# Kernel tuning notes

Hardware: AMD Instinct MI355X
Metric: run time of the kernel (lower is better)

## Reference

```python
import jax, jax.numpy as jnp
import numpy as np

SE, SD, B = 400, 50, 32
H, IN, A = 512, 512, 128
VF, V = 1024, 32000

def _p(k, shape):
    return jax.random.normal(k, shape, dtype=jnp.float32) * 0.02

def setup_inputs() -> dict:
    key = jax.random.key(0)
    ks = jax.random.split(key, 24)
    inp = {
        'output_enc': jax.random.normal(ks[0], (SE, B, 2 * H), dtype=jnp.float32),
        'input_dec': jax.random.normal(ks[1], (SD, B, IN), dtype=jnp.float32),
        'hidden_enc': jax.random.normal(ks[2], (4, B, H), dtype=jnp.float32),
        'cell_state_enc': jax.random.normal(ks[3], (4, B, H), dtype=jnp.float32),
        # LSTM layer 0 (PyTorch gate order i,f,g,o)
        'W_ih0': _p(ks[4], (4 * H, IN)), 'W_hh0': _p(ks[5], (4 * H, H)),
        'b_ih0': _p(ks[6], (4 * H,)), 'b_hh0': _p(ks[7], (4 * H,)),
        # LSTM layer 1
        'W_ih1': _p(ks[8], (4 * H, H)), 'W_hh1': _p(ks[9], (4 * H, H)),
        'b_ih1': _p(ks[10], (4 * H,)), 'b_hh1': _p(ks[11], (4 * H,)),
        # reduce_dim: 2H -> H
        'W_red': _p(ks[12], (H, 2 * H)), 'b_red': _p(ks[13], (H,)),
        # attention: 3H -> A, attn_out: A -> 1 (no bias)
        'W_att': _p(ks[14], (A, 3 * H)), 'b_att': _p(ks[15], (A,)),
        'v_att': _p(ks[16], (1, A)),
        # vocab MLP: 3H -> VF -> V
        'W_v1': _p(ks[17], (VF, 3 * H)), 'b_v1': _p(ks[18], (VF,)),
        'W_v2': _p(ks[19], (V, VF)), 'b_v2': _p(ks[20], (V,)),
    }
    return inp

def _forward(output_enc, input_dec, hidden_enc, cell_state_enc,
             W_ih0, W_hh0, b_ih0, b_hh0, W_ih1, W_hh1, b_ih1, b_hh1,
             W_red, b_red, W_att, b_att, v_att, W_v1, b_v1, W_v2, b_v2):
    # first_word=True path: fold bidirectional encoder state [4,B,H] -> [2,B,2H] -> [2,B,H]
    old_enc = jnp.concatenate([hidden_enc[0:2], hidden_enc[2:]], axis=-1)
    old_cell = jnp.concatenate([cell_state_enc[0:2], cell_state_enc[2:]], axis=-1)
    new_enc = old_enc @ W_red.T + b_red    # [2,B,H]
    new_cell = old_cell @ W_red.T + b_red  # [2,B,H]

    def lstm_cell(x, h, c, W_ih, W_hh, b_ih, b_hh):
        g = x @ W_ih.T + h @ W_hh.T + b_ih + b_hh
        i, f, gg, o = jnp.split(g, 4, axis=-1)
        c_new = jax.nn.sigmoid(f) * c + jax.nn.sigmoid(i) * jnp.tanh(gg)
        h_new = jax.nn.sigmoid(o) * jnp.tanh(c_new)
        return h_new, c_new

    def step(carry, x_t):
        h0, c0, h1, c1 = carry
        h0, c0 = lstm_cell(x_t, h0, c0, W_ih0, W_hh0, b_ih0, b_hh0)
        h1, c1 = lstm_cell(h0, h1, c1, W_ih1, W_hh1, b_ih1, b_hh1)
        return (h0, c0, h1, c1), h1

    init = (new_enc[0], new_cell[0], new_enc[1], new_cell[1])
    (h0f, c0f, h1f, c1f), output_dec = jax.lax.scan(step, init, input_dec)
    hidden_dec = jnp.stack([h0f, h1f])       # [2,B,H]
    cell_state_dec = jnp.stack([c0f, c1f])   # [2,B,H]

    # Additive (Bahdanau) attention, batched over all decoder timesteps.
    # cat order is (output_enc, output_dec) -> first 2H cols of W_att hit encoder.
    enc_part = output_enc @ W_att[:, :2 * H].T              # [Se,B,A]
    dec_part = output_dec @ W_att[:, 2 * H:].T + b_att       # [Sd,B,A]
    e = jnp.tanh(enc_part[:, None] + dec_part[None])         # [Se,Sd,B,A]
    e = jnp.einsum('stba,a->stb', e, v_att[0])               # [Se,Sd,B]
    attn = jax.nn.softmax(e, axis=0)                         # softmax over encoder dim
    context = jnp.einsum('stb,sbe->tbe', attn, output_enc)   # [Sd,B,2H]

    pv_in = jnp.concatenate([output_dec, context], axis=-1)  # [Sd,B,3H]
    pvocab = (pv_in @ W_v1.T + b_v1) @ W_v2.T + b_v2         # [Sd,B,V]
    return pvocab, (hidden_dec, cell_state_dec)

def reference(output_enc, input_dec, hidden_enc, cell_state_enc,
              W_ih0, W_hh0, b_ih0, b_hh0, W_ih1, W_hh1, b_ih1, b_hh1,
              W_red, b_red, W_att, b_att, v_att, W_v1, b_v1, W_v2, b_v2):
    return _forward(output_enc, input_dec, hidden_enc, cell_state_enc,
                    W_ih0, W_hh0, b_ih0, b_hh0, W_ih1, W_hh1, b_ih1, b_hh1,
                    W_red, b_red, W_att, b_att, v_att, W_v1, b_v1, W_v2, b_v2)
```

## Files before the change

### kernel.cpp

```cpp
#include <hip/hip_runtime.h>
#include <cstdint>

#define DEV __device__ __forceinline__

typedef short bfrag __attribute__((ext_vector_type(8)));
typedef float ffrag __attribute__((ext_vector_type(4)));

constexpr int SE = 400, SD = 50, BB = 32;
constexpr int HH = 512, INW = 512, AA = 128;
constexpr int VF = 1024, VV = 32000;
constexpr int G4 = 2048;

DEV ushort f2bf(float f) {
    uint32_t u = __float_as_uint(f);
    u = (u + 0x7FFF + ((u >> 16) & 1)) >> 16;
    return (ushort)u;
}
DEV float bf2f(ushort u) { return __uint_as_float(((uint32_t)u) << 16); }
DEV float sigm_(float x) { return 1.f / (1.f + __expf(-x)); }
DEV float tanh_(float x) { float e = __expf(2.f * x); return 1.f - 2.f / (e + 1.f); }
DEV int imin(int a, int b) { return a < b ? a : b; }

DEV void gload_lds16(const void* g, void* l) {
    __builtin_amdgcn_global_load_lds((const __attribute__((address_space(1))) uint32_t*)g,
                                     (__attribute__((address_space(3))) uint32_t*)l, 16, 0, 0);
}

struct CvtFlatTab {
    const float* src[6];
    ushort* dst[6];
    int blk_end[6];
    int nseg;
};
__global__ __launch_bounds__(256) void k_cvt_multi(CvtFlatTab t) {
    int blk = blockIdx.x, seg = 0;
    while (seg < t.nseg - 1 && blk >= t.blk_end[seg]) seg++;
    int base = seg ? t.blk_end[seg - 1] : 0;
    long i = (long)(blk - base) * 256 + threadIdx.x;
    float4 v = ((const float4*)t.src[seg])[i];
    ushort4 o;
    o.x = f2bf(v.x); o.y = f2bf(v.y); o.z = f2bf(v.z); o.w = f2bf(v.w);
    ((ushort4*)t.dst[seg])[i] = o;
}

struct CvtStrTab {
    const float* src[4];
    ushort* dst[4];
    int ss[4], so[4], ds[4], dofs[4], c4n[4];
    int blk_end[4];
    int nseg;
};
__global__ __launch_bounds__(256) void k_cvt_str_multi(CvtStrTab t) {
    int blk = blockIdx.x, seg = 0;
    while (seg < t.nseg - 1 && blk >= t.blk_end[seg]) seg++;
    int base = seg ? t.blk_end[seg - 1] : 0;
    int i = (blk - base) * 256 + threadIdx.x;
    int c4n = t.c4n[seg];
    int r = i / c4n, c = (i - r * c4n) * 4;
    float4 v = *(const float4*)(t.src[seg] + (size_t)r * t.ss[seg] + t.so[seg] + c);
    ushort4 o;
    o.x = f2bf(v.x); o.y = f2bf(v.y); o.z = f2bf(v.z); o.w = f2bf(v.w);
    *(ushort4*)(t.dst[seg] + (size_t)r * t.ds[seg] + t.dofs[seg] + c) = o;
}

__global__ __launch_bounds__(256) void k_bsum(const float* __restrict__ bi0, const float* __restrict__ bh0,
                                              const float* __restrict__ bi1, const float* __restrict__ bh1,
                                              float* __restrict__ bsum0, float* __restrict__ bsum1) {
    int i = blockIdx.x * 256 + threadIdx.x;
    if (i >= G4) return;
    bsum0[i] = bi0[i] + bh0[i];
    bsum1[i] = bi1[i] + bh1[i];
}

__global__ __launch_bounds__(256) void k_fold(const float* __restrict__ hid,
                                              const float* __restrict__ cel,
                                              const float* __restrict__ W_red,
                                              const float* __restrict__ b_red,
                                              float* __restrict__ h0m,
                                              float* __restrict__ c0, float* __restrict__ c1,
                                              ushort* __restrict__ AB) {
    int tid = threadIdx.x;
    int j = blockIdx.x * 256 + tid;
    int b = blockIdx.y;
    int l = blockIdx.z & 1;
    bool is_c = blockIdx.z >> 1;
    const float* src = is_c ? cel : hid;
    __shared__ float xs[1024];
    for (int i = tid; i < 512; i += 256) {
        xs[i]       = src[((size_t)l * BB + b) * HH + i];
        xs[512 + i] = src[((size_t)(l + 2) * BB + b) * HH + i];
    }
    __syncthreads();
    const float4* w  = (const float4*)(W_red + (size_t)j * 1024);
    const float4* xv = (const float4*)xs;
    float acc = b_red[j];
    for (int k = 0; k < 256; k++) {
        float4 a = w[k], x = xv[k];
        acc += a.x * x.x + a.y * x.y + a.z * x.z + a.w * x.w;
    }
    if (is_c) {
        (l ? c1 : c0)[(size_t)b * HH + j] = acc;
    } else {
        if (l == 0) {
            h0m[(size_t)b * HH + j] = acc;
            AB[(size_t)32 * 1024 + (size_t)b * 1024 + j] = f2bf(acc);
        } else {
            AB[(size_t)b * 1024 + 512 + j] = f2bf(acc);
        }
    }
}

__global__ __launch_bounds__(256) void k_cell(const ushort* __restrict__ Aprev,
                                              const ushort* __restrict__ W0,
                                              const ushort* __restrict__ W1,
                                              const float* __restrict__ gx,
                                              const float* __restrict__ bsum1,
                                              float* __restrict__ c0, float* __restrict__ c1,
                                              float* __restrict__ h0m,
                                              float* __restrict__ od1,
                                              ushort* __restrict__ od1_bf,
                                              ushort* __restrict__ x1row,
                                              ushort* __restrict__ ABdst,
                                              int do_l0, int do_l1) {
    const int layer = blockIdx.y;
    if (layer == 0 && !do_l0) return;
    if (layer == 1 && !do_l1) return;
    const int jb = blockIdx.x;
    const int tid = threadIdx.x, wave = tid >> 6, lane = tid & 63;
    const int lr = lane & 15, lk = lane >> 4;
    const int K = layer ? 1024 : 512;
    const ushort* Wm = layer ? W1 : W0;
    const int wstride = layer ? 1024 : 512;
    const int n0 = wave * 512 + jb * 16;

    const ushort* arow0 = Aprev + (size_t)lr * 1024;
    const ushort* arow1 = Aprev + (size_t)(16 + lr) * 1024;
    const ushort* wrow  = Wm + (size_t)(n0 + lr) * wstride;

    ffrag acc0 = {0.f, 0.f, 0.f, 0.f}, acc1 = {0.f, 0.f, 0.f, 0.f};
    #pragma unroll 4
    for (int k0 = 0; k0 < K; k0 += 32) {
        bfrag a0 = *(const bfrag*)(arow0 + k0 + lk * 8);
        bfrag a1 = *(const bfrag*)(arow1 + k0 + lk * 8);
        bfrag bw = *(const bfrag*)(wrow + k0 + lk * 8);
        acc0 = __builtin_amdgcn_mfma_f32_16x16x32_bf16(a0, bw, acc0, 0, 0, 0);
        acc1 = __builtin_amdgcn_mfma_f32_16x16x32_bf16(a1, bw, acc1, 0, 0, 0);
    }

    __shared__ float gl[4][32][16];
    #pragma unroll
    for (int r = 0; r < 4; r++) {
        gl[wave][lk * 4 + r][lr]      = acc0[r];
        gl[wave][16 + lk * 4 + r][lr] = acc1[r];
    }
    __syncthreads();

    for (int e = tid; e < 512; e += 256) {
        int b = e >> 4, jj = e & 15;
        int j = jb * 16 + jj;
        float gi = gl[0][b][jj], gf = gl[1][b][jj], gg = gl[2][b][jj], go = gl[3][b][jj];
        if (layer == 0) {
            const float* gxp = gx + (size_t)b * G4;
            gi += gxp[j]; gf += gxp[512 + j]; gg += gxp[1024 + j]; go += gxp[1536 + j];
        } else {
            gi += bsum1[j]; gf += bsum1[512 + j]; gg += bsum1[1024 + j]; go += bsum1[1536 + j];
        }
        float* cc = layer ? c1 : c0;
        size_t ci = (size_t)b * HH + j;
        float cn = sigm_(gf) * cc[ci] + sigm_(gi) * tanh_(gg);
        cc[ci] = cn;
        float hn = sigm_(go) * tanh_(cn);
        ushort hb = f2bf(hn);
        if (layer == 0) {
            h0m[ci] = hn;
            ABdst[(size_t)b * 1024 + j] = hb;
        } else {
            od1[ci] = hn;
            od1_bf[ci] = hb;
            x1row[(size_t)b * 1536 + j] = hb;
            ABdst[(size_t)b * 1024 + 512 + j] = hb;
        }
    }
}

__global__ __launch_bounds__(256) void k_states(const float* __restrict__ h0,
                                                const float* __restrict__ h1,
                                                const float* __restrict__ c0,
                                                const float* __restrict__ c1,
                                                float* __restrict__ out) {
    int i = blockIdx.x * 256 + threadIdx.x;
    if (i >= BB * HH) return;
    out[i]               = h0[i];
    out[BB * HH + i]     = h1[i];
    out[2 * BB * HH + i] = c0[i];
    out[3 * BB * HH + i] = c1[i];
}

template <int OUT_BF16>
__global__ __launch_bounds__(256) void k_gemm128(const ushort* __restrict__ X,
                                                 const ushort* __restrict__ W,
                                                 float* __restrict__ Cf,
                                                 ushort* __restrict__ Cb,
                                                 const float* __restrict__ bias,
                                                 int M, int N, int K, int nmt) {
    __shared__ ushort As[2][4096];
    __shared__ ushort Bs[2][4096];
    const int tid = threadIdx.x;
    const int wave = tid >> 6, lane = tid & 63;
    const int lr = lane & 15, lk = lane >> 4;
    const int wm = wave >> 1, wn = wave & 1;

    int nwg = gridDim.x, flat = blockIdx.x;
    int q = nwg >> 3, r = nwg & 7;
    int xcd = flat & 7, idx = flat >> 3;
    int wg = (xcd < r ? xcd * (q + 1) : r * (q + 1) + (xcd - r) * q) + idx;
    const int m0 = (wg % nmt) * 128, n0 = (wg / nmt) * 128;

    ffrag acc[4][4];
    #pragma unroll
    for (int i = 0; i < 4; i++)
        #pragma unroll
        for (int j = 0; j < 4; j++) acc[i][j] = (ffrag){0.f, 0.f, 0.f, 0.f};

    const int srow = wave * 16 + (lane >> 2);
    const int scol = (lane & 3) * 8;
    const int ar0 = imin(m0 + srow, M - 1);
    const int ar1 = imin(m0 + 64 + srow, M - 1);
    const ushort* Agp0 = X + (size_t)ar0 * K + scol;
    const ushort* Agp1 = X + (size_t)ar1 * K + scol;
    const ushort* Bgp0 = W + (size_t)(n0 + srow) * K + scol;
    const ushort* Bgp1 = W + (size_t)(n0 + 64 + srow) * K + scol;

    auto stage = [&](int buf, int k0) {
        ushort* AsW = As[buf] + wave * 512;
        ushort* BsW = Bs[buf] + wave * 512;
        gload_lds16(Agp0 + k0, AsW);
        gload_lds16(Agp1 + k0, AsW + 2048);
        gload_lds16(Bgp0 + k0, BsW);
        gload_lds16(Bgp1 + k0, BsW + 2048);
    };
    auto compute = [&](int buf) {
        bfrag a[4], bfr[4];
        #pragma unroll
        for (int mf = 0; mf < 4; mf++)
            a[mf] = *(const bfrag*)&As[buf][(wm * 64 + mf * 16 + lr) * 32 + lk * 8];
        #pragma unroll
        for (int nf = 0; nf < 4; nf++)
            bfr[nf] = *(const bfrag*)&Bs[buf][(wn * 64 + nf * 16 + lr) * 32 + lk * 8];
        #pragma unroll
        for (int mf = 0; mf < 4; mf++)
            #pragma unroll
            for (int nf = 0; nf < 4; nf++)
                acc[mf][nf] = __builtin_amdgcn_mfma_f32_16x16x32_bf16(a[mf], bfr[nf], acc[mf][nf], 0, 0, 0);
    };

    const int nt = K >> 5;
    stage(0, 0);
    __syncthreads();
    int cur = 0;
    for (int t = 0; t < nt - 1; ++t) {
        stage(cur ^ 1, (t + 1) << 5);
        compute(cur);
        __syncthreads();
        cur ^= 1;
    }
    compute(cur);

    #pragma unroll
    for (int mf = 0; mf < 4; mf++) {
        int rbase = m0 + wm * 64 + mf * 16 + lk * 4;
        #pragma unroll
        for (int nf = 0; nf < 4; nf++) {
            int cc = n0 + wn * 64 + nf * 16 + lr;
            float bv = bias ? bias[cc] : 0.f;
            #pragma unroll
            for (int rr = 0; rr < 4; rr++) {
                int row = rbase + rr;
                if (row < M) {
                    float v = acc[mf][nf][rr] + bv;
                    if (OUT_BF16) Cb[(size_t)row * N + cc] = f2bf(v);
                    else          Cf[(size_t)row * N + cc] = v;
                }
            }
        }
    }
}

__global__ __launch_bounds__(256) void k_scores(const float* __restrict__ encp,
                                                const float* __restrict__ decp,
                                                const float* __restrict__ v_att,
                                                float* __restrict__ attn) {
    int t = blockIdx.x, b = blockIdx.y, tid = threadIdx.x;
    __shared__ float dp[128], vv[128];
    __shared__ float e_lds[400];
    __shared__ float red[8];
    if (tid < 128) {
        dp[tid] = decp[((size_t)t * BB + b) * AA + tid];
        vv[tid] = v_att[tid];
    }
    __syncthreads();
    const float4* dp4 = (const float4*)dp;
    const float4* vv4 = (const float4*)vv;
    for (int s = tid; s < SE; s += 256) {
        const float4* ep4 = (const float4*)(encp + ((size_t)s * BB + b) * AA);
        float a0 = 0.f;
        #pragma unroll 4
        for (int a = 0; a < AA / 4; a++) {
            float4 e = ep4[a], d = dp4[a], v = vv4[a];
            a0 += v.x * tanh_(e.x + d.x) + v.y * tanh_(e.y + d.y)
                + v.z * tanh_(e.z + d.z) + v.w * tanh_(e.w + d.w);
        }
        e_lds[s] = a0;
    }
    __syncthreads();
    float m = -1e30f;
    for (int s = tid; s < SE; s += 256) m = fmaxf(m, e_lds[s]);
    #pragma unroll
    for (int o = 32; o > 0; o >>= 1) m = fmaxf(m, __shfl_xor(m, o));
    if ((tid & 63) == 0) red[tid >> 6] = m;
    __syncthreads();
    m = fmaxf(fmaxf(red[0], red[1]), fmaxf(red[2], red[3]));
    float sum = 0.f;
    for (int s = tid; s < SE; s += 256) {
        float ex = __expf(e_lds[s] - m);
        e_lds[s] = ex;
        sum += ex;
    }
    #pragma unroll
    for (int o = 32; o > 0; o >>= 1) sum += __shfl_xor(sum, o);
    if ((tid & 63) == 0) red[4 + (tid >> 6)] = sum;
    __syncthreads();
    float inv = 1.f / (red[4] + red[5] + red[6] + red[7]);
    for (int s = tid; s < SE; s += 256)
        attn[((size_t)b * SD + t) * SE + s] = e_lds[s] * inv;
}

__global__ __launch_bounds__(256) void k_context(const float* __restrict__ attn,
                                                 const ushort* __restrict__ oe_bf,
                                                 ushort* __restrict__ x1) {
    int b = blockIdx.x, nc = blockIdx.y, th = blockIdx.z, tid = threadIdx.x;
    __shared__ float at[25][400];
    const float* ap = attn + ((size_t)b * SD + th * 25) * SE;
    for (int i = tid; i < 25 * 400; i += 256) at[i / 400][i % 400] = ap[i];
    __syncthreads();
    int n = nc * 256 + tid;
    float acc[25];
    #pragma unroll
    for (int i = 0; i < 25; i++) acc[i] = 0.f;
    for (int s = 0; s < SE; s += 4) {
        float v0 = bf2f(oe_bf[((size_t)(s + 0) * BB + b) * 1024 + n]);
        float v1 = bf2f(oe_bf[((size_t)(s + 1) * BB + b) * 1024 + n]);
        float v2 = bf2f(oe_bf[((size_t)(s + 2) * BB + b) * 1024 + n]);
        float v3 = bf2f(oe_bf[((size_t)(s + 3) * BB + b) * 1024 + n]);
        #pragma unroll
        for (int tt = 0; tt < 25; tt++)
            acc[tt] += at[tt][s] * v0 + at[tt][s + 1] * v1
                     + at[tt][s + 2] * v2 + at[tt][s + 3] * v3;
    }
    #pragma unroll
    for (int tt = 0; tt < 25; tt++) {
        int row = (th * 25 + tt) * BB + b;
        x1[(size_t)row * 1536 + 512 + n] = f2bf(acc[tt]);
    }
}

extern "C" void kernel_launch(void* const* d_in, const int* in_sizes, int n_in,
                              void* d_out, int out_size, void* d_ws, size_t ws_size,
                              hipStream_t stream) {
    const float* output_enc = (const float*)d_in[0];
    const float* input_dec  = (const float*)d_in[1];
    const float* hidden_enc = (const float*)d_in[2];
    const float* cell_enc   = (const float*)d_in[3];
    const float* W_ih0 = (const float*)d_in[4],  *W_hh0 = (const float*)d_in[5];
    const float* b_ih0 = (const float*)d_in[6],  *b_hh0 = (const float*)d_in[7];
    const float* W_ih1 = (const float*)d_in[8],  *W_hh1 = (const float*)d_in[9];
    const float* b_ih1 = (const float*)d_in[10], *b_hh1 = (const float*)d_in[11];
    const float* W_red = (const float*)d_in[12], *b_red = (const float*)d_in[13];
    const float* W_att = (const float*)d_in[14], *b_att = (const float*)d_in[15];
    const float* v_att = (const float*)d_in[16];
    const float* W_v1  = (const float*)d_in[17], *b_v1 = (const float*)d_in[18];
    const float* W_v2  = (const float*)d_in[19], *b_v2 = (const float*)d_in[20];

    char* ws = (char*)d_ws;
    size_t off = 0;
    auto alloc = [&](size_t bytes) -> void* {
        void* p = ws + off;
        off += (bytes + 255) & ~(size_t)255;
        return p;
    };
    float*  h0m    = (float*)alloc(BB * HH * 4);
    float*  c0     = (float*)alloc(BB * HH * 4);
    float*  c1     = (float*)alloc(BB * HH * 4);
    ushort* AB     = (ushort*)alloc(2 * BB * 1024 * 2);
    float*  od     = (float*)alloc((size_t)SD * BB * HH * 4);
    ushort* od_bf  = (ushort*)alloc((size_t)SD * BB * HH * 2);
    ushort* xd_bf  = (ushort*)alloc((size_t)SD * BB * INW * 2);
    ushort* wih0b  = (ushort*)alloc((size_t)G4 * 512 * 2);
    ushort* whh0b  = (ushort*)alloc((size_t)G4 * 512 * 2);
    ushort* w1cat  = (ushort*)alloc((size_t)G4 * 1024 * 2);
    float*  bsum0  = (float*)alloc(G4 * 4);
    float*  bsum1  = (float*)alloc(G4 * 4);
    float*  gx0    = (float*)alloc((size_t)SD * BB * G4 * 4);
    ushort* oe_bf  = (ushort*)alloc((size_t)SE * BB * 1024 * 2);
    ushort* wae    = (ushort*)alloc((size_t)AA * 1024 * 2);
    ushort* wad    = (ushort*)alloc((size_t)AA * 512 * 2);
    float*  encp   = (float*)alloc((size_t)SE * BB * AA * 4);
    float*  decp   = (float*)alloc((size_t)SD * BB * AA * 4);
    float*  attn   = (float*)alloc((size_t)BB * SD * SE * 4);
    ushort* x1     = (ushort*)alloc((size_t)1600 * 1536 * 2);
    ushort* wv1    = (ushort*)alloc((size_t)VF * 1536 * 2);
    ushort* y1     = (ushort*)alloc((size_t)1600 * VF * 2);
    ushort* wv2    = (ushort*)alloc((size_t)VV * 1024 * 2);

    {
        CvtFlatTab t;
        int nb = 0, k = 0;
        auto add = [&](const float* s, ushort* d, long n) {
            t.src[k] = s; t.dst[k] = d; nb += (int)(n / 1024); t.blk_end[k] = nb; k++;
        };
        add(input_dec, xd_bf, (long)SD * BB * INW);
        add(output_enc, oe_bf, (long)SE * BB * 1024);
        add(W_ih0, wih0b, (long)G4 * 512);
        add(W_hh0, whh0b, (long)G4 * 512);
        add(W_v1, wv1, (long)VF * 1536);
        add(W_v2, wv2, (long)VV * 1024);
        t.nseg = k;
        k_cvt_multi<<<nb, 256, 0, stream>>>(t);
    }
    {
        CvtStrTab t;
        int nb = 0, k = 0;
        auto add = [&](const float* s, ushort* d, int rows, int cols, int ss, int so, int ds, int dofs) {
            t.src[k] = s; t.dst[k] = d; t.ss[k] = ss; t.so[k] = so;
            t.ds[k] = ds; t.dofs[k] = dofs; t.c4n[k] = cols / 4;
            nb += rows * cols / 1024; t.blk_end[k] = nb; k++;
        };
        add(W_ih1, w1cat, G4, 512, 512, 0, 1024, 0);
        add(W_hh1, w1cat, G4, 512, 512, 0, 1024, 512);
        add(W_att, wae, AA, 1024, 1536, 0, 1024, 0);
        add(W_att, wad, AA, 512, 1536, 1024, 512, 0);
        t.nseg = k;
        k_cvt_str_multi<<<nb, 256, 0, stream>>>(t);
    }
    k_bsum<<<8, 256, 0, stream>>>(b_ih0, b_hh0, b_ih1, b_hh1, bsum0, bsum1);

    k_fold<<<dim3(2, 32, 4), 256, 0, stream>>>(hidden_enc, cell_enc, W_red, b_red,
                                               h0m, c0, c1, AB);

    k_gemm128<0><<<13 * 16, 256, 0, stream>>>(xd_bf, wih0b, gx0, nullptr, bsum0,
                                              SD * BB, G4, 512, 13);

    for (int i = 0; i <= SD; i++) {
        const ushort* Aprev = AB + (size_t)((i + 1) & 1) * BB * 1024;
        ushort* ABdst = AB + (size_t)(i & 1) * BB * 1024;
        int t1c = (i > 0) ? (i - 1) : 0;
        k_cell<<<dim3(32, 2), 256, 0, stream>>>(Aprev, whh0b, w1cat,
                                                gx0 + (size_t)i * BB * G4, bsum1,
                                                c0, c1, h0m,
                                                od + (size_t)t1c * BB * HH,
                                                od_bf + (size_t)t1c * BB * HH,
                                                x1 + (size_t)t1c * BB * 1536,
                                                ABdst, (int)(i < SD), (int)(i > 0));
    }
    k_states<<<64, 256, 0, stream>>>(h0m, od + (size_t)(SD - 1) * BB * HH, c0, c1,
                                     (float*)d_out + (size_t)SD * BB * VV);

    k_gemm128<0><<<100, 256, 0, stream>>>(oe_bf, wae, encp, nullptr,
                                          (const float*)nullptr, SE * BB, AA, 1024, 100);
    k_gemm128<0><<<13, 256, 0, stream>>>(od_bf, wad, decp, nullptr,
                                         b_att, SD * BB, AA, 512, 13);
    k_scores<<<dim3(SD, BB), 256, 0, stream>>>(encp, decp, v_att, attn);
    k_context<<<dim3(32, 4, 2), 256, 0, stream>>>(attn, oe_bf, x1);

    k_gemm128<1><<<13 * 8, 256, 0, stream>>>(x1, wv1, nullptr, y1, b_v1,
                                             1600, VF, 1536, 13);
    k_gemm128<0><<<13 * 250, 256, 0, stream>>>(y1, wv2, (float*)d_out, nullptr, b_v2,
                                               1600, VV, 1024, 13);
    (void)in_sizes; (void)n_in; (void)out_size; (void)ws_size;
}
```

Baseline: 1.631 ms.

## Fuse per-step LSTM cell launches into one persistent cooperative kernel

Replaces 51 separate k_cell launches plus the k_states copy kernel with one cooperative kernel that loops over time steps and uses grid.sync between them. It targets the kernel launch and inter-launch gap overhead of the sequential LSTM recurrence. In exchange it relies on cooperative launch support and pays a grid-wide barrier each step. It also enlarges the gx0 buffer by one step so the unused layer-0 pointer at i=SD stays in bounds.

```diff
diff --git a/kernel.cpp b/kernel.cpp
--- a/kernel.cpp
+++ b/kernel.cpp
@@ -1,5 +1,8 @@
 #include <hip/hip_runtime.h>
+#include <hip/hip_cooperative_groups.h>
 #include <cstdint>
+
+namespace cg = cooperative_groups;
 
 #define DEV __device__ __forceinline__
 
@@ -110,21 +113,18 @@
     }
 }
 
-__global__ __launch_bounds__(256) void k_cell(const ushort* __restrict__ Aprev,
-                                              const ushort* __restrict__ W0,
-                                              const ushort* __restrict__ W1,
-                                              const float* __restrict__ gx,
-                                              const float* __restrict__ bsum1,
-                                              float* __restrict__ c0, float* __restrict__ c1,
-                                              float* __restrict__ h0m,
-                                              float* __restrict__ od1,
-                                              ushort* __restrict__ od1_bf,
-                                              ushort* __restrict__ x1row,
-                                              ushort* __restrict__ ABdst,
-                                              int do_l0, int do_l1) {
+__global__ __launch_bounds__(256) void k_lstm_persist(ushort* AB,
+                                                      const ushort* __restrict__ W0,
+                                                      const ushort* __restrict__ W1,
+                                                      const float* __restrict__ gx0,
+                                                      const float* __restrict__ bsum1,
+                                                      float* c0, float* c1,
+                                                      float* h0m,
+                                                      float* od, ushort* od_bf,
+                                                      ushort* x1,
+                                                      float* out_states) {
+    cg::grid_group grid = cg::this_grid();
     const int layer = blockIdx.y;
-    if (layer == 0 && !do_l0) return;
-    if (layer == 1 && !do_l1) return;
     const int jb = blockIdx.x;
     const int tid = threadIdx.x, wave = tid >> 6, lane = tid & 63;
     const int lr = lane & 15, lk = lane >> 4;
@@ -132,68 +132,73 @@
     const ushort* Wm = layer ? W1 : W0;
     const int wstride = layer ? 1024 : 512;
     const int n0 = wave * 512 + jb * 16;
-
-    const ushort* arow0 = Aprev + (size_t)lr * 1024;
-    const ushort* arow1 = Aprev + (size_t)(16 + lr) * 1024;
-    const ushort* wrow  = Wm + (size_t)(n0 + lr) * wstride;
-
-    ffrag acc0 = {0.f, 0.f, 0.f, 0.f}, acc1 = {0.f, 0.f, 0.f, 0.f};
-    #pragma unroll 4
-    for (int k0 = 0; k0 < K; k0 += 32) {
-        bfrag a0 = *(const bfrag*)(arow0 + k0 + lk * 8);
-        bfrag a1 = *(const bfrag*)(arow1 + k0 + lk * 8);
-        bfrag bw = *(const bfrag*)(wrow + k0 + lk * 8);
-        acc0 = __builtin_amdgcn_mfma_f32_16x16x32_bf16(a0, bw, acc0, 0, 0, 0);
-        acc1 = __builtin_amdgcn_mfma_f32_16x16x32_bf16(a1, bw, acc1, 0, 0, 0);
-    }
+    const ushort* wrow = Wm + (size_t)(n0 + lr) * wstride;
 
     __shared__ float gl[4][32][16];
-    #pragma unroll
-    for (int r = 0; r < 4; r++) {
-        gl[wave][lk * 4 + r][lr]      = acc0[r];
-        gl[wave][16 + lk * 4 + r][lr] = acc1[r];
-    }
-    __syncthreads();
-
-    for (int e = tid; e < 512; e += 256) {
-        int b = e >> 4, jj = e & 15;
-        int j = jb * 16 + jj;
-        float gi = gl[0][b][jj], gf = gl[1][b][jj], gg = gl[2][b][jj], go = gl[3][b][jj];
-        if (layer == 0) {
-            const float* gxp = gx + (size_t)b * G4;
-            gi += gxp[j]; gf += gxp[512 + j]; gg += gxp[1024 + j]; go += gxp[1536 + j];
-        } else {
-            gi += bsum1[j]; gf += bsum1[512 + j]; gg += bsum1[1024 + j]; go += bsum1[1536 + j];
+
+    for (int i = 0; i <= SD; ++i) {
+        const bool active = layer ? (i > 0) : (i < SD);
+        if (active) {
+            const ushort* Aprev = AB + (size_t)((i + 1) & 1) * BB * 1024;
+            ushort* ABdst = AB + (size_t)(i & 1) * BB * 1024;
+            const int t1c = (i > 0) ? (i - 1) : 0;
+            const float* gx = gx0 + (size_t)i * BB * G4;
+            const ushort* arow0 = Aprev + (size_t)lr * 1024;
+            const ushort* arow1 = Aprev + (size_t)(16 + lr) * 1024;
+
+            ffrag acc0 = {0.f, 0.f, 0.f, 0.f}, acc1 = {0.f, 0.f, 0.f, 0.f};
+            #pragma unroll 4
+            for (int k0 = 0; k0 < K; k0 += 32) {
+                bfrag a0 = *(const bfrag*)(arow0 + k0 + lk * 8);
+                bfrag a1 = *(const bfrag*)(arow1 + k0 + lk * 8);
+                bfrag bw = *(const bfrag*)(wrow + k0 + lk * 8);
+                acc0 = __builtin_amdgcn_mfma_f32_16x16x32_bf16(a0, bw, acc0, 0, 0, 0);
+                acc1 = __builtin_amdgcn_mfma_f32_16x16x32_bf16(a1, bw, acc1, 0, 0, 0);
+            }
+
+            #pragma unroll
+            for (int r = 0; r < 4; r++) {
+                gl[wave][lk * 4 + r][lr]      = acc0[r];
+                gl[wave][16 + lk * 4 + r][lr] = acc1[r];
+            }
+            __syncthreads();
+
+            for (int e = tid; e < 512; e += 256) {
+                int b = e >> 4, jj = e & 15;
+                int j = jb * 16 + jj;
+                float gi = gl[0][b][jj], gf = gl[1][b][jj], gg = gl[2][b][jj], go = gl[3][b][jj];
+                if (layer == 0) {
+                    const float* gxp = gx + (size_t)b * G4;
+                    gi += gxp[j]; gf += gxp[512 + j]; gg += gxp[1024 + j]; go += gxp[1536 + j];
+                } else {
+                    gi += bsum1[j]; gf += bsum1[512 + j]; gg += bsum1[1024 + j]; go += bsum1[1536 + j];
+                }
+                float* cc = layer ? c1 : c0;
+                size_t ci = (size_t)b * HH + j;
+                float cn = sigm_(gf) * cc[ci] + sigm_(gi) * tanh_(gg);
+                cc[ci] = cn;
+                float hn = sigm_(go) * tanh_(cn);
+                ushort hb = f2bf(hn);
+                if (layer == 0) {
+                    h0m[ci] = hn;
+                    ABdst[(size_t)b * 1024 + j] = hb;
+                } else {
+                    od[(size_t)t1c * BB * HH + ci] = hn;
+                    od_bf[(size_t)t1c * BB * HH + ci] = hb;
+                    x1[((size_t)t1c * BB + b) * 1536 + j] = hb;
+                    ABdst[(size_t)b * 1024 + 512 + j] = hb;
+                }
+            }
         }
-        float* cc = layer ? c1 : c0;
-        size_t ci = (size_t)b * HH + j;
-        float cn = sigm_(gf) * cc[ci] + sigm_(gi) * tanh_(gg);
-        cc[ci] = cn;
-        float hn = sigm_(go) * tanh_(cn);
-        ushort hb = f2bf(hn);
-        if (layer == 0) {
-            h0m[ci] = hn;
-            ABdst[(size_t)b * 1024 + j] = hb;
-        } else {
-            od1[ci] = hn;
-            od1_bf[ci] = hb;
-            x1row[(size_t)b * 1536 + j] = hb;
-            ABdst[(size_t)b * 1024 + 512 + j] = hb;
-        }
-    }
-}
-
-__global__ __launch_bounds__(256) void k_states(const float* __restrict__ h0,
-                                                const float* __restrict__ h1,
-                                                const float* __restrict__ c0,
-                                                const float* __restrict__ c1,
-                                                float* __restrict__ out) {
-    int i = blockIdx.x * 256 + threadIdx.x;
-    if (i >= BB * HH) return;
-    out[i]               = h0[i];
-    out[BB * HH + i]     = h1[i];
-    out[2 * BB * HH + i] = c0[i];
-    out[3 * BB * HH + i] = c1[i];
+        __threadfence();
+        grid.sync();
+    }
+
+    int g = (blockIdx.y * 32 + blockIdx.x) * 256 + tid;
+    out_states[g]                = h0m[g];
+    out_states[BB * HH + g]      = od[(size_t)(SD - 1) * BB * HH + g];
+    out_states[2 * BB * HH + g]  = c0[g];
+    out_states[3 * BB * HH + g]  = c1[g];
 }
 
 template <int OUT_BF16>
@@ -400,7 +405,7 @@
     ushort* w1cat  = (ushort*)alloc((size_t)G4 * 1024 * 2);
     float*  bsum0  = (float*)alloc(G4 * 4);
     float*  bsum1  = (float*)alloc(G4 * 4);
-    float*  gx0    = (float*)alloc((size_t)SD * BB * G4 * 4);
+    float*  gx0    = (float*)alloc((size_t)(SD + 1) * BB * G4 * 4);
     ushort* oe_bf  = (ushort*)alloc((size_t)SE * BB * 1024 * 2);
     ushort* wae    = (ushort*)alloc((size_t)AA * 1024 * 2);
     ushort* wad    = (ushort*)alloc((size_t)AA * 512 * 2);
@@ -450,20 +455,13 @@
     k_gemm128<0><<<13 * 16, 256, 0, stream>>>(xd_bf, wih0b, gx0, nullptr, bsum0,
                                               SD * BB, G4, 512, 13);
 
-    for (int i = 0; i <= SD; i++) {
-        const ushort* Aprev = AB + (size_t)((i + 1) & 1) * BB * 1024;
-        ushort* ABdst = AB + (size_t)(i & 1) * BB * 1024;
-        int t1c = (i > 0) ? (i - 1) : 0;
-        k_cell<<<dim3(32, 2), 256, 0, stream>>>(Aprev, whh0b, w1cat,
-                                                gx0 + (size_t)i * BB * G4, bsum1,
-                                                c0, c1, h0m,
-                                                od + (size_t)t1c * BB * HH,
-                                                od_bf + (size_t)t1c * BB * HH,
-                                                x1 + (size_t)t1c * BB * 1536,
-                                                ABdst, (int)(i < SD), (int)(i > 0));
-    }
-    k_states<<<64, 256, 0, stream>>>(h0m, od + (size_t)(SD - 1) * BB * HH, c0, c1,
-                                     (float*)d_out + (size_t)SD * BB * VV);
+    {
+        float* out_states = (float*)d_out + (size_t)SD * BB * VV;
+        void* params[] = { &AB, &whh0b, &w1cat, &gx0, &bsum1,
+                           &c0, &c1, &h0m, &od, &od_bf, &x1, &out_states };
+        hipLaunchCooperativeKernel((const void*)k_lstm_persist, dim3(32, 2), dim3(256),
+                                   params, 0, stream);
+    }
 
     k_gemm128<0><<<100, 256, 0, stream>>>(oe_bf, wae, encp, nullptr,
                                           (const float*)nullptr, SE * BB, AA, 1024, 100);
```

Result: slower. 2.261 ms (+38.6%).
